# Optimization experiments

Hardware: AMD Instinct MI355X
Metric: run time of the kernel (lower is better)

Reference implementation:

```python
import jax, jax.numpy as jnp
import numpy as np

N_ATOMS = 50000   # nAtoms
KMAX = 32         # max neighbors per atom
EMB_ATOM = 256    # emb_size_atom
EMB_PAIR_IN = 64  # emb_size_pair_in
EMB_PAIR_OUT = 64 # emb_size_pair_out
EMB_RBF = 16      # emb_size_rbf
INV_SQRT = lambda n: 1.0 / np.sqrt(n).astype(np.float32)


def setup_inputs() -> dict:
    key = jax.random.key(0)
    k_h, k_rb, k_src, k_wd, k_wb, k_wu = jax.random.split(key, 6)
    h = jax.random.normal(k_h, (N_ATOMS, EMB_ATOM), dtype=jnp.float32)
    rad_basis = jax.random.normal(k_rb, (N_ATOMS, EMB_RBF, KMAX), dtype=jnp.float32)
    # each destination atom has exactly KMAX neighbors -> unique (dst, slot) pairs
    dst = jnp.repeat(jnp.arange(N_ATOMS, dtype=jnp.int64), KMAX)
    src = jax.random.randint(k_src, (N_ATOMS * KMAX,), 0, N_ATOMS, dtype=jnp.int64)
    edge_index = jnp.stack([src, dst])  # (2, nEdges)
    target_neighbor_idx = jnp.tile(jnp.arange(KMAX, dtype=jnp.int64), N_ATOMS)
    W_down = jax.random.normal(k_wd, (EMB_ATOM, EMB_PAIR_IN), dtype=jnp.float32) * INV_SQRT(EMB_ATOM)
    W_bilinear = jax.random.normal(k_wb, (EMB_RBF * EMB_PAIR_IN, EMB_PAIR_OUT), dtype=jnp.float32) * INV_SQRT(EMB_RBF * EMB_PAIR_IN)
    W_up = jax.random.normal(k_wu, (EMB_PAIR_OUT, EMB_ATOM), dtype=jnp.float32) * INV_SQRT(EMB_PAIR_OUT)
    return {"h": h, "rad_basis": rad_basis, "edge_index": edge_index,
            "target_neighbor_idx": target_neighbor_idx,
            "W_down": W_down, "W_bilinear": W_bilinear, "W_up": W_up}


def reference(h, rad_basis, edge_index, target_neighbor_idx, W_down, W_bilinear, W_up):
    num_atoms = h.shape[0]
    kmax = rad_basis.shape[-1]
    # down projection (no bias, no activation)
    x_b = h @ W_down                               # (nAtoms, emb_pair_in)
    x_ba = x_b[edge_index[0]]                      # (nEdges, emb_pair_in) gather from source atoms
    # scatter into dense padded tensor (nAtoms, Kmax, emb_pair_in)
    x2 = jnp.zeros((num_atoms, kmax, x_ba.shape[-1]), dtype=x_ba.dtype)
    x2 = x2.at[edge_index[1], target_neighbor_idx].set(x_ba)
    # per-atom batched matmul with radial basis: (nAtoms, emb_rbf, Kmax) @ (nAtoms, Kmax, emb_pair_in)
    x_ba2 = jnp.einsum('nrk,nkp->nrp', rad_basis, x2)
    # bilinear projection on flattened (emb_rbf * emb_pair_in); ScaleFactor default scale = 1.0 (identity)
    h_out = x_ba2.reshape(num_atoms, -1) @ W_bilinear  # (nAtoms, emb_pair_out)
    return h_out @ W_up                               # (nAtoms, emb_size_atom)
```

## Files before the change

### kernel.cpp

```cpp
#include <hip/hip_runtime.h>

#define N_ATOMS 50000
#define KMAX 32
#define EMB_ATOM 256
#define EP_IN 64
#define EP_OUT 64
#define EMB_RBF 16
#define NEDGES (N_ATOMS * KMAX)

typedef _Float16 half_t;
typedef __attribute__((ext_vector_type(2))) _Float16 half2_t;
typedef __attribute__((ext_vector_type(4))) _Float16 half4_t;
typedef __attribute__((ext_vector_type(8))) _Float16 half8_t;
typedef __attribute__((ext_vector_type(4))) float f32x4;

static_assert(N_ATOMS % 16 == 0, "fused kernel assumes 16 atoms per block");

#define GLOAD_LDS16(g, l)                                                     \
    __builtin_amdgcn_global_load_lds(                                         \
        (const __attribute__((address_space(1))) void*)(g),                   \
        (__attribute__((address_space(3))) void*)(l), 16, 0, 0)

#define PW_WD 64
#define PW_WB 256
#define PW_WU 64
#define PREP_W_NB (PW_WD + PW_WB + PW_WU + 1)

#define XB2_NB 782
#define SC_NB (NEDGES / 256)
#define PREP_MAIN_NB (XB2_NB + SC_NB)

__global__ __launch_bounds__(256) void prep_w(const float* __restrict__ Wd,
                                              const float* __restrict__ Wb,
                                              const float* __restrict__ Wu,
                                              half_t* __restrict__ Wd2,
                                              half_t* __restrict__ Wb2,
                                              half_t* __restrict__ Wu2,
                                              half_t* __restrict__ zrow) {
    const int bid = blockIdx.x;
    const int t = threadIdx.x;
    if (bid < PW_WD) {
        int i = bid * 256 + t;
        int e = i & 7, lv = (i >> 3) & 63, s = (i >> 9) & 7, nt = i >> 12;
        int c = lv & 15, g = lv >> 4;
        int k = s * 32 + g * 8 + e;
        int n = nt * 16 + c;
        Wd2[i] = (half_t)Wd[(size_t)k * 64 + n];
    } else if (bid < PW_WD + PW_WB) {
        int i = (bid - PW_WD) * 256 + t;
        int e = i & 7, lv = (i >> 3) & 63;
        int c = lv & 15, g = lv >> 4;
        int kh = (i >> 13) & 1, ot = i >> 14;
        int o = ot * 16 + c;
        int idx = kh * 512 + ((i >> 9) & 15) * 32 + g * 8 + e;
        int r = ((idx >> 6) & 3) * 4 + (idx & 3);
        int p = (idx >> 8) * 16 + ((idx >> 2) & 15);
        Wb2[i] = (half_t)Wb[(size_t)(r * 64 + p) * 64 + o];
    } else if (bid < PW_WD + PW_WB + PW_WU) {
        int i = (bid - PW_WD - PW_WB) * 256 + t;
        int e = i & 7, lv = (i >> 3) & 63;
        int c = lv & 15, g = lv >> 4;
        int kk = (i >> 9) & 1, nt = (i >> 10) & 1, w = i >> 11;
        int oc = w * 32 + nt * 16 + c;
        int o = kk * 32 + g * 8 + e;
        Wu2[i] = (half_t)Wu[(size_t)o * 256 + oc];
    } else {
        if (t < 128) zrow[t] = (half_t)0.f;
    }
}

__global__ __launch_bounds__(256) void prep_main(const float* __restrict__ h,
                                                 const int*   __restrict__ ei,
                                                 const int*   __restrict__ tni,
                                                 const half_t* __restrict__ Wd2,
                                                 half_t* __restrict__ xbh,
                                                 int*    __restrict__ sidx) {
    const int bid = blockIdx.x;
    const int t = threadIdx.x;
    if (bid < XB2_NB) {
        const int w = t >> 6, l = t & 63;
        const int c = l & 15, g = l >> 4;
        const int r0 = bid * 64 + w * 16;
        const f32x4 fzero = {0.f, 0.f, 0.f, 0.f};
        f32x4 acc[4] = {fzero, fzero, fzero, fzero};

        int row_ld = r0 + c;
        if (row_ld > N_ATOMS - 1) row_ld = N_ATOMS - 1;
        const float* hrow = h + (size_t)row_ld * 256;

        #pragma unroll
        for (int s = 0; s < 8; ++s) {
            f32x4 h0 = *reinterpret_cast<const f32x4*>(hrow + s * 32 + g * 8);
            f32x4 h1 = *reinterpret_cast<const f32x4*>(hrow + s * 32 + g * 8 + 4);
            half8_t af;
            #pragma unroll
            for (int j = 0; j < 4; ++j) { af[j] = (half_t)h0[j]; af[4 + j] = (half_t)h1[j]; }
            #pragma unroll
            for (int nt = 0; nt < 4; ++nt) {
                half8_t bf = *reinterpret_cast<const half8_t*>(
                    &Wd2[(size_t)(nt * 8 + s) * 512 + l * 8]);
                acc[nt] = __builtin_amdgcn_mfma_f32_16x16x32_f16(af, bf, acc[nt], 0, 0, 0);
            }
        }
        #pragma unroll
        for (int nt = 0; nt < 4; ++nt)
            #pragma unroll
            for (int i = 0; i < 4; ++i) {
                int row = r0 + g * 4 + i;
                if (row < N_ATOMS)
                    xbh[(size_t)row * 64 + nt * 16 + c] = (half_t)acc[nt][i];
            }
    } else {
        int i = (bid - XB2_NB) * 256 + t;
        int s = ei[i];
        int d = ei[NEDGES + i];
        int k = tni[i];
        sidx[d * KMAX + k] = s;
    }
}

__device__ __forceinline__ void consume_batch(const char* stb, int c, int g,
                                              half4_t radf, half4_t ident,
                                              f32x4 (&acc)[4]) {
    const f32x4 fzero = {0.f, 0.f, 0.f, 0.f};
    #pragma unroll
    for (int pc = 0; pc < 4; ++pc) {
        int slot = (pc * 2 + (g >> 1)) ^ (c & 7);
        half4_t gf = *reinterpret_cast<const half4_t*>(
            stb + c * 128 + slot * 16 + (g & 1) * 8);
        f32x4 tD = __builtin_amdgcn_mfma_f32_16x16x16f16(gf, ident, fzero, 0, 0, 0);
        half4_t b2;
        #pragma unroll
        for (int j = 0; j < 4; ++j) b2[j] = (half_t)tD[j];
        acc[pc] = __builtin_amdgcn_mfma_f32_16x16x16f16(radf, b2, acc[pc], 0, 0, 0);
    }
}

#define ISSUE(as, kc, bufb) do {                                              \
    _Pragma("unroll")                                                         \
    for (int h_ = 0; h_ < 2; ++h_) {                                          \
        int s_ = __shfl(sv, (as) * 32 + (kc) * 16 + h_ * 8 + (l >> 3), 64);   \
        const half_t* src_ = ((unsigned)s_ < (unsigned)N_ATOMS)               \
            ? (xbh + (size_t)s_ * 64) : zrow;                                 \
        src_ += (((l & 7) ^ (l >> 3)) << 3);          \
        GLOAD_LDS16(src_, (half_t*)(Rbase + (bufb)) + h_ * 512);              \
    }                                                                         \
} while (0)

#define WRITE_ATOM(a_, accv) do {                                             \
    _Pragma("unroll")                                                         \
    for (int pc = 0; pc < 4; ++pc) {                                          \
        half4_t hv;                                                           \
        _Pragma("unroll")                                                     \
        for (int j = 0; j < 4; ++j) hv[j] = (half_t)accv[pc][j];              \
        int byte_ = ((a_) * 2048 + pc * 512 + g * 128 + c * 8) ^              \
                    (((a_) & 7) << 4);                                        \
        *reinterpret_cast<half4_t*>(reinterpret_cast<char*>(xba2s) + byte_) = hv; \
    }                                                                         \
} while (0)

#define WAIT_VM(n) do {                                                       \
    asm volatile("s_waitcnt vmcnt(" #n ")" ::: "memory");                     \
    __builtin_amdgcn_sched_barrier(0);                                        \
} while (0)

#define WAIT_LGKM() do {                                                      \
    asm volatile("s_waitcnt lgkmcnt(0)" ::: "memory");                        \
    __builtin_amdgcn_sched_barrier(0);                                        \
} while (0)

#define SBAR() __builtin_amdgcn_sched_barrier(0)

__global__ __launch_bounds__(512, 6) void fused(const half_t* __restrict__ xbh,
                                                const float*  __restrict__ rad,
                                                const int*    __restrict__ sidxg,
                                                const half_t* __restrict__ Wb2,
                                                const half_t* __restrict__ Wu2,
                                                const half_t* __restrict__ zrow,
                                                float* __restrict__ out) {
    __shared__ __align__(16) half_t xba2s[16 * 1024];
    __shared__ __align__(16) float  preds[2 * 16 * 68];
    __shared__ __align__(16) half_t houts[16 * 64];

    const int t = threadIdx.x;
    const int w = t >> 6;
    const int l = t & 63;
    const int c = l & 15;
    const int g = l >> 4;
    const int a0 = blockIdx.x * 16;

    char* Rbase = reinterpret_cast<char*>(xba2s) + w * 4096;

    const f32x4 fzero = {0.f, 0.f, 0.f, 0.f};

    int sv = sidxg[(size_t)(a0 + w * 2) * KMAX + l];
    const float* radw = &rad[(size_t)(a0 + w * 2) * 512];
    f32x4 rv[4];
    #pragma unroll
    for (int q = 0; q < 4; ++q)
        rv[q] = *reinterpret_cast<const f32x4*>(radw + q * 256 + l * 4);

    ISSUE(0, 0, 0);
    ISSUE(0, 1, 2048);
    SBAR();

    const int ot = w >> 1, kh = w & 1;
    const half_t* wbbase = &Wb2[(size_t)((ot * 2 + kh) * 16) * 512];
    half8_t bfr[4];
    #pragma unroll
    for (int j = 0; j < 4; ++j)
        bfr[j] = *reinterpret_cast<const half8_t*>(wbbase + j * 512 + l * 8);
    SBAR();

    half4_t radF[2][2];
    #pragma unroll
    for (int as = 0; as < 2; ++as)
        #pragma unroll
        for (int kc = 0; kc < 2; ++kc) {
            int srcl = (c & 7) * 8 + kc * 4 + g;
            #pragma unroll
            for (int j = 0; j < 4; ++j) {
                float lo = __shfl(rv[as * 2 + 0][j], srcl, 64);
                float hi = __shfl(rv[as * 2 + 1][j], srcl, 64);
                radF[as][kc][j] = (half_t)((c & 8) ? hi : lo);
            }
        }

    half4_t ident;
    #pragma unroll
    for (int j = 0; j < 4; ++j) ident[j] = (half_t)((g * 4 + j == c) ? 1.0f : 0.0f);

    f32x4 acc0[4] = {fzero, fzero, fzero, fzero};
    f32x4 acc1[4] = {fzero, fzero, fzero, fzero};

    WAIT_VM(6);
    consume_batch(Rbase, c, g, radF[0][0], ident, acc0);
    WAIT_LGKM();
    ISSUE(1, 0, 0);
    WAIT_VM(6);
    consume_batch(Rbase + 2048, c, g, radF[0][1], ident, acc0);
    WAIT_LGKM();
    ISSUE(1, 1, 2048);
    WAIT_VM(2);
    consume_batch(Rbase, c, g, radF[1][0], ident, acc1);
    WRITE_ATOM(w * 2, acc0);
    WAIT_VM(0);
    consume_batch(Rbase + 2048, c, g, radF[1][1], ident, acc1);
    WRITE_ATOM(w * 2 + 1, acc1);

    __syncthreads();

    {
        f32x4 acc2[4] = {fzero, fzero, fzero, fzero};
        #pragma unroll
        for (int j = 0; j < 16; ++j) {
            int abyte = (c * 2048 + (kh * 512 + j * 32) * 2 + g * 16) ^ ((c & 7) << 4);
            half8_t af = *reinterpret_cast<const half8_t*>(
                reinterpret_cast<const char*>(xba2s) + abyte);
            half8_t bf = bfr[j & 3];
            if (j + 4 < 16)
                bfr[j & 3] = *reinterpret_cast<const half8_t*>(wbbase + (j + 4) * 512 + l * 8);
            acc2[j & 3] = __builtin_amdgcn_mfma_f32_16x16x32_f16(af, bf, acc2[j & 3], 0, 0, 0);
        }
        f32x4 accT = acc2[0] + acc2[1] + acc2[2] + acc2[3];
        #pragma unroll
        for (int i = 0; i < 4; ++i)
            preds[kh * 1088 + (g * 4 + i) * 68 + ot * 16 + c] = accT[i];
    }

    half8_t wuf[2][2];
    #pragma unroll
    for (int nt = 0; nt < 2; ++nt)
        #pragma unroll
        for (int kk = 0; kk < 2; ++kk)
            wuf[nt][kk] = *reinterpret_cast<const half8_t*>(
                &Wu2[(size_t)(((w * 2 + nt) * 2 + kk) * 64 + l) * 8]);

    __syncthreads();

    {
        int m = t >> 5, oj = (t & 31) << 1;
        float s0 = preds[m * 68 + oj]     + preds[1088 + m * 68 + oj];
        float s1 = preds[m * 68 + oj + 1] + preds[1088 + m * 68 + oj + 1];
        half2_t hv; hv[0] = (half_t)s0; hv[1] = (half_t)s1;
        int byte_ = (m * 128 + oj * 2) ^ ((m & 7) << 4);
        *reinterpret_cast<half2_t*>(reinterpret_cast<char*>(houts) + byte_) = hv;
    }
    __syncthreads();

    half8_t ha[2];
    #pragma unroll
    for (int kk = 0; kk < 2; ++kk) {
        int byte_ = (c * 128 + kk * 64 + g * 16) ^ ((c & 7) << 4);
        ha[kk] = *reinterpret_cast<const half8_t*>(
            reinterpret_cast<const char*>(houts) + byte_);
    }
    #pragma unroll
    for (int nt = 0; nt < 2; ++nt) {
        int oc0 = w * 32 + nt * 16;
        f32x4 acc3 = fzero;
        acc3 = __builtin_amdgcn_mfma_f32_16x16x32_f16(ha[0], wuf[nt][0], acc3, 0, 0, 0);
        acc3 = __builtin_amdgcn_mfma_f32_16x16x32_f16(ha[1], wuf[nt][1], acc3, 0, 0, 0);
        #pragma unroll
        for (int i = 0; i < 4; ++i)
            out[(size_t)(a0 + g * 4 + i) * 256 + oc0 + c] = acc3[i];
    }
}

extern "C" void kernel_launch(void* const* d_in, const int* in_sizes, int n_in,
                              void* d_out, int out_size, void* d_ws, size_t ws_size,
                              hipStream_t stream) {
    const float* h   = (const float*)d_in[0];
    const float* rad = (const float*)d_in[1];
    const int*   ei  = (const int*)d_in[2];
    const int*   tni = (const int*)d_in[3];
    const float* Wd  = (const float*)d_in[4];
    const float* Wb  = (const float*)d_in[5];
    const float* Wu  = (const float*)d_in[6];
    float* out = (float*)d_out;

    half_t* xbh  = (half_t*)d_ws;
    int*    sidx = (int*)((char*)d_ws + (size_t)N_ATOMS * EP_IN * sizeof(half_t));
    half_t* Wb2  = (half_t*)((char*)sidx + (size_t)NEDGES * sizeof(int));
    half_t* Wu2  = Wb2 + 64 * 1024;
    half_t* Wd2  = Wu2 + 16384;
    half_t* zrow = Wd2 + 16384;

    prep_w<<<PREP_W_NB, 256, 0, stream>>>(Wd, Wb, Wu, Wd2, Wb2, Wu2, zrow);
    prep_main<<<PREP_MAIN_NB, 256, 0, stream>>>(h, ei, tni, Wd2, xbh, sidx);
    fused<<<N_ATOMS / 16, 512, 0, stream>>>(xbh, rad, sidx, Wb2, Wu2, zrow, out);
}
```

Measured before the change: 74.60 us.

## Drop houts staging pass and prefetch bilinear/up weights before barrier

Removes the separate LDS stage that summed the two K-half partials into a half-precision buffer, along with one __syncthreads. Each wave now reads both fp32 partial sums directly from preds and builds its MFMA A-fragments in registers. The Wb prefetch depth is doubled to 8 fragments and the Wu loads are hoisted ahead of the barrier. s_setprio is raised around the MFMA loops. The cost is more VGPRs, which could threaten the 6-blocks-per-CU occupancy target, and the unpadded float4 reads from preds may cause LDS bank conflicts.

```diff
diff --git a/kernel.cpp b/kernel.cpp
--- a/kernel.cpp
+++ b/kernel.cpp
@@ -180,7 +180,6 @@
                                                 float* __restrict__ out) {
     __shared__ __align__(16) half_t xba2s[16 * 1024];
     __shared__ __align__(16) float  preds[2 * 16 * 68];
-    __shared__ __align__(16) half_t houts[16 * 64];
 
     const int t = threadIdx.x;
     const int w = t >> 6;
@@ -206,7 +205,7 @@
 
     const int ot = w >> 1, kh = w & 1;
     const half_t* wbbase = &Wb2[(size_t)((ot * 2 + kh) * 16) * 512];
-    half8_t bfr[4];
+    half8_t bfr[8];
     #pragma unroll
     for (int j = 0; j < 4; ++j)
         bfr[j] = *reinterpret_cast<const half8_t*>(wbbase + j * 512 + l * 8);
@@ -248,62 +247,66 @@
     consume_batch(Rbase + 2048, c, g, radF[1][1], ident, acc1);
     WRITE_ATOM(w * 2 + 1, acc1);
 
+    #pragma unroll
+    for (int j = 4; j < 8; ++j)
+        bfr[j] = *reinterpret_cast<const half8_t*>(wbbase + j * 512 + l * 8);
+    half8_t wuf[2][2];
+    #pragma unroll
+    for (int nt = 0; nt < 2; ++nt)
+        #pragma unroll
+        for (int kk = 0; kk < 2; ++kk)
+            wuf[nt][kk] = *reinterpret_cast<const half8_t*>(
+                &Wu2[(size_t)(((w * 2 + nt) * 2 + kk) * 64 + l) * 8]);
+
     __syncthreads();
 
     {
         f32x4 acc2[4] = {fzero, fzero, fzero, fzero};
+        __builtin_amdgcn_s_setprio(1);
         #pragma unroll
         for (int j = 0; j < 16; ++j) {
             int abyte = (c * 2048 + (kh * 512 + j * 32) * 2 + g * 16) ^ ((c & 7) << 4);
             half8_t af = *reinterpret_cast<const half8_t*>(
                 reinterpret_cast<const char*>(xba2s) + abyte);
-            half8_t bf = bfr[j & 3];
-            if (j + 4 < 16)
-                bfr[j & 3] = *reinterpret_cast<const half8_t*>(wbbase + (j + 4) * 512 + l * 8);
+            half8_t bf = bfr[j & 7];
+            if (j < 8)
+                bfr[j] = *reinterpret_cast<const half8_t*>(wbbase + (j + 8) * 512 + l * 8);
             acc2[j & 3] = __builtin_amdgcn_mfma_f32_16x16x32_f16(af, bf, acc2[j & 3], 0, 0, 0);
         }
+        __builtin_amdgcn_s_setprio(0);
         f32x4 accT = acc2[0] + acc2[1] + acc2[2] + acc2[3];
         #pragma unroll
         for (int i = 0; i < 4; ++i)
             preds[kh * 1088 + (g * 4 + i) * 68 + ot * 16 + c] = accT[i];
     }
-
-    half8_t wuf[2][2];
-    #pragma unroll
-    for (int nt = 0; nt < 2; ++nt)
-        #pragma unroll
-        for (int kk = 0; kk < 2; ++kk)
-            wuf[nt][kk] = *reinterpret_cast<const half8_t*>(
-                &Wu2[(size_t)(((w * 2 + nt) * 2 + kk) * 64 + l) * 8]);
-
     __syncthreads();
 
-    {
-        int m = t >> 5, oj = (t & 31) << 1;
-        float s0 = preds[m * 68 + oj]     + preds[1088 + m * 68 + oj];
-        float s1 = preds[m * 68 + oj + 1] + preds[1088 + m * 68 + oj + 1];
-        half2_t hv; hv[0] = (half_t)s0; hv[1] = (half_t)s1;
-        int byte_ = (m * 128 + oj * 2) ^ ((m & 7) << 4);
-        *reinterpret_cast<half2_t*>(reinterpret_cast<char*>(houts) + byte_) = hv;
-    }
-    __syncthreads();
-
     half8_t ha[2];
     #pragma unroll
     for (int kk = 0; kk < 2; ++kk) {
-        int byte_ = (c * 128 + kk * 64 + g * 16) ^ ((c & 7) << 4);
-        ha[kk] = *reinterpret_cast<const half8_t*>(
-            reinterpret_cast<const char*>(houts) + byte_);
-    }
-    #pragma unroll
-    for (int nt = 0; nt < 2; ++nt) {
-        int oc0 = w * 32 + nt * 16;
-        f32x4 acc3 = fzero;
-        acc3 = __builtin_amdgcn_mfma_f32_16x16x32_f16(ha[0], wuf[nt][0], acc3, 0, 0, 0);
-        acc3 = __builtin_amdgcn_mfma_f32_16x16x32_f16(ha[1], wuf[nt][1], acc3, 0, 0, 0);
-        #pragma unroll
-        for (int i = 0; i < 4; ++i)
-            out[(size_t)(a0 + g * 4 + i) * 256 + oc0 + c] = acc3[i];
+        const float* p0 = &preds[c * 68 + kk * 32 + g * 8];
+        f32x4 x0 = *reinterpret_cast<const f32x4*>(p0);
+        f32x4 x1 = *reinterpret_cast<const f32x4*>(p0 + 4);
+        f32x4 y0 = *reinterpret_cast<const f32x4*>(p0 + 1088);
+        f32x4 y1 = *reinterpret_cast<const f32x4*>(p0 + 1092);
+        #pragma unroll
+        for (int j = 0; j < 4; ++j) {
+            ha[kk][j]     = (half_t)(x0[j] + y0[j]);
+            ha[kk][4 + j] = (half_t)(x1[j] + y1[j]);
+        }
+    }
+    __builtin_amdgcn_s_setprio(1);
+    f32x4 acc3a = fzero, acc3b = fzero;
+    acc3a = __builtin_amdgcn_mfma_f32_16x16x32_f16(ha[0], wuf[0][0], acc3a, 0, 0, 0);
+    acc3a = __builtin_amdgcn_mfma_f32_16x16x32_f16(ha[1], wuf[0][1], acc3a, 0, 0, 0);
+    acc3b = __builtin_amdgcn_mfma_f32_16x16x32_f16(ha[0], wuf[1][0], acc3b, 0, 0, 0);
+    acc3b = __builtin_amdgcn_mfma_f32_16x16x32_f16(ha[1], wuf[1][1], acc3b, 0, 0, 0);
+    __builtin_amdgcn_s_setprio(0);
+    #pragma unroll
+    for (int i = 0; i < 4; ++i) {
+        int row = a0 + g * 4 + i;
+        out[(size_t)row * 256 + w * 32 + c] = acc3a[i];
+        out[(size_t)row * 256 + w * 32 + 16 + c] = acc3b[i];
     }
 }
 
```

After: 87.71 us. 1.18x slower.
